# Kernel tuning notes

Hardware: AMD Instinct MI355X
Metric: run time of the kernel (lower is better)

The kernel has to match this reference:

```python
import jax, jax.numpy as jnp
import numpy as np

B, N, D, H = 8, 2048, 512, 8  # batch, seq (incl. CLS), emb_dim, heads


def setup_inputs() -> dict:
    key = jax.random.key(0)
    kx, km, k1, k2, k3, k4 = jax.random.split(key, 6)
    x = jax.random.normal(kx, (B, N, D), dtype=jnp.float32)
    # mask covers the N-1 non-CLS tokens; forward pads a leading True for CLS
    mask = jax.random.bernoulli(km, p=0.9, shape=(B, N - 1))
    s = 0.02
    Wqkv = jax.random.normal(k1, (D, 3 * D), dtype=jnp.float32) * s
    bqkv = jax.random.normal(k2, (3 * D,), dtype=jnp.float32) * s
    Wout = jax.random.normal(k3, (D, D), dtype=jnp.float32) * s
    bout = jax.random.normal(k4, (D,), dtype=jnp.float32) * s
    return {"x": x, "mask": mask, "Wqkv": Wqkv, "bqkv": bqkv,
            "Wout": Wout, "bout": bout, "num_heads": H}


def reference(x, mask, Wqkv, bqkv, Wout, bout, num_heads):
    b, n, d = x.shape
    h = num_heads
    dh = d // h
    scale = d ** (-0.5)  # NOTE: module scales by emb_dim^-0.5, not head_dim^-0.5

    qkv = x @ Wqkv + bqkv                      # [b, n, 3d]
    q, k, v = jnp.split(qkv, 3, axis=-1)
    def to_heads(t):
        return t.reshape(b, n, h, dh).transpose(0, 2, 1, 3)  # [b, h, n, dh]
    q, k, v = map(to_heads, (q, k, v))

    scores = jnp.einsum('bhqd,bhkd->bhqk', q, k) * scale     # [b, h, n, n]

    # pad leading True for CLS token, then outer-product pair mask
    m = jnp.pad(mask, ((0, 0), (1, 0)), constant_values=True)  # [b, n]
    pair = m[:, None, :, None] & m[:, None, None, :]           # [b, 1, n, n]
    neg = jnp.asarray(-1e9, dtype=scores.dtype)  # finite stand-in for -inf (avoids NaN rows)
    scores = jnp.where(pair, scores, neg)

    attn = jax.nn.softmax(scores, axis=-1)
    out = jnp.einsum('bhqk,bhkd->bhqd', attn, v)               # [b, h, n, dh]
    out = out.transpose(0, 2, 1, 3).reshape(b, n, d)
    return out @ Wout + bout
```

## Files before the change

kernel.cpp:

```cpp
#include <hip/hip_runtime.h>
#include <math.h>

#define BB  8
#define SEQ 2048
#define EMB 512
#define NH  8
#define DH  64
#define NBH (BB * NH)
#define MROWS (BB * SEQ)
#define QKV_ELEMS ((size_t)NBH * SEQ * DH)
#define MASK_ELEMS (BB * (SEQ - 1))
#define QSCALE 0.06375871307545f

typedef __attribute__((ext_vector_type(8)))  short short8;
typedef __attribute__((ext_vector_type(4)))  float float4e;
typedef __attribute__((ext_vector_type(16))) float float16e;
typedef __attribute__((ext_vector_type(4)))  unsigned int uint4e;
typedef __attribute__((ext_vector_type(2)))  unsigned int uint2e;
typedef unsigned short ushort_t;

static __device__ inline unsigned short f2bf(float f) {
    unsigned int u = __float_as_uint(f);
    unsigned int r = (u + 0x7fffu + ((u >> 16) & 1u)) >> 16;
    return (unsigned short)r;
}

static __device__ inline void gl_lds16(const unsigned short* g, unsigned short* l) {
    __builtin_amdgcn_global_load_lds(
        (const __attribute__((address_space(1))) void*)g,
        (__attribute__((address_space(3))) void*)l, 16, 0, 0);
}

#define PREP_CONV   8192
#define PREP_MASK   (PREP_CONV + 64)
#define PREP_WQ     (PREP_MASK + (1536 / 32) * (EMB / 32))
#define PREP_TOTAL  (PREP_WQ + (EMB / 32) * (EMB / 32))

__global__ __launch_bounds__(256) void prep(const float* __restrict__ x,
                                            const void* __restrict__ mraw,
                                            const float* __restrict__ Wqkv,
                                            const float* __restrict__ Wout,
                                            ushort_t* __restrict__ xb,
                                            float* __restrict__ pmf,
                                            float* __restrict__ mkl,
                                            float* __restrict__ zrow,
                                            ushort_t* __restrict__ wqt,
                                            ushort_t* __restrict__ wot) {
    __shared__ float T[32][33];
    __shared__ int flag;
    const int bid = blockIdx.x;
    const int tid = threadIdx.x;

    if (bid < PREP_CONV) {
        const size_t i = ((size_t)bid * 256 + tid) * 4;
        float4 v = *(const float4*)&x[i];
        ushort4 o;
        o.x = f2bf(v.x); o.y = f2bf(v.y); o.z = f2bf(v.z); o.w = f2bf(v.w);
        *(ushort4*)&xb[i] = o;
    } else if (bid < PREP_MASK) {
        if (tid == 0) flag = 0;
        __syncthreads();
        const unsigned int* mi = (const unsigned int*)mraw;
        int local = 0;
        for (int i = tid; i < MASK_ELEMS / 4; i += 256) {
            if (mi[i] > 1u) local = 1;
        }
        if (local) flag = 1;
        __syncthreads();
        const int isbyte = flag;
        const unsigned char* mb = (const unsigned char*)mraw;
        const int* m32 = (const int*)mraw;
        const int i = (bid - PREP_CONV) * 256 + tid;
        const int b = i >> 11, n = i & (SEQ - 1);
        int v;
        if (n == 0) v = 1;
        else {
            const int src = b * (SEQ - 1) + n - 1;
            v = isbyte ? (int)mb[src] : (m32[src] != 0 ? 1 : 0);
        }
        pmf[i] = v ? 1.0f : 0.0f;
        mkl[i] = v ? 0.0f : -1e9f;
        if (i < SEQ) zrow[i] = 0.0f;
    } else {
        const float* src;
        ushort_t* dst;
        int N, idx;
        if (bid < PREP_WQ) {
            src = Wqkv; dst = wqt; N = 1536; idx = bid - PREP_MASK;
        } else {
            src = Wout; dst = wot; N = EMB; idx = bid - PREP_WQ;
        }
        const int nb = N / 32;
        const int n0 = (idx % nb) * 32;
        const int k0 = (idx / nb) * 32;
        {
            const int r = tid >> 3, c4 = (tid & 7) * 4;
            *(float4*)&T[r][c4] = *(const float4*)&src[(size_t)(k0 + r) * N + n0 + c4];
        }
        __syncthreads();
        const int n = tid >> 3, k4 = (tid & 7) * 4;
        ushort4 hv;
        hv.x = f2bf(T[k4 + 0][n]);
        hv.y = f2bf(T[k4 + 1][n]);
        hv.z = f2bf(T[k4 + 2][n]);
        hv.w = f2bf(T[k4 + 3][n]);
        *(ushort4*)&dst[(size_t)(n0 + n) * EMB + k0 + k4] = hv;
    }
}

__global__ __launch_bounds__(256) void qkv_mfma(const ushort_t* __restrict__ xb,
                                                const ushort_t* __restrict__ wt,
                                                const float* __restrict__ bias,
                                                ushort_t* __restrict__ qb,
                                                ushort_t* __restrict__ kb,
                                                ushort_t* __restrict__ vt) {
    __shared__ __align__(16) ushort_t As[128 * 32];
    __shared__ __align__(16) ushort_t Bs[128 * 32];
    const int tid  = threadIdx.x;
    const int w    = tid >> 6;
    const int lane = tid & 63;
    const int l16  = lane & 15;
    const int quad = lane >> 4;
    const int wq   = w >> 1;
    const int wn   = w & 1;
    const int row0 = blockIdx.y * 128;
    const int col0 = blockIdx.x * 128;

    float4e acc[4][4];
    #pragma unroll
    for (int i = 0; i < 4; ++i)
        #pragma unroll
        for (int j = 0; j < 4; ++j) acc[i][j] = (float4e){0.f, 0.f, 0.f, 0.f};

    const int srow = tid >> 2;
    const int csrc = (tid & 3) ^ (srow & 3);

    for (int k0 = 0; k0 < EMB; k0 += 32) {
        #pragma unroll
        for (int s = 0; s < 2; ++s) {
            const int row = s * 64 + srow;
            gl_lds16(xb + (size_t)(row0 + row) * EMB + k0 + csrc * 8,
                     As + s * 2048 + w * 512);
            gl_lds16(wt + (size_t)(col0 + row) * EMB + k0 + csrc * 8,
                     Bs + s * 2048 + w * 512);
        }
        __syncthreads();
        short8 af[4], bf[4];
        #pragma unroll
        for (int mt = 0; mt < 4; ++mt) {
            const int rm = wq * 64 + mt * 16 + l16;
            af[mt] = *(const short8*)(As + rm * 32 + ((quad ^ (rm & 3)) * 8));
        }
        #pragma unroll
        for (int nt = 0; nt < 4; ++nt) {
            const int rn = wn * 64 + nt * 16 + l16;
            bf[nt] = *(const short8*)(Bs + rn * 32 + ((quad ^ (rn & 3)) * 8));
        }
        #pragma unroll
        for (int mt = 0; mt < 4; ++mt)
            #pragma unroll
            for (int nt = 0; nt < 4; ++nt)
                acc[mt][nt] = __builtin_amdgcn_mfma_f32_16x16x32_bf16(af[mt], bf[nt], acc[mt][nt], 0, 0, 0);
        __syncthreads();
    }

    #pragma unroll
    for (int nt = 0; nt < 4; ++nt) {
        const int cb    = col0 + wn * 64 + nt * 16;
        const int which = cb >> 9;
        const int h     = (cb >> 6) & 7;
        const int dcol  = (cb & 63) + l16;
        const float bz  = bias[cb + l16];
        if (which == 2) {
            #pragma unroll
            for (int mt = 0; mt < 4; ++mt) {
                const int rg = row0 + wq * 64 + mt * 16 + quad * 4;
                const int b = rg >> 11, n = rg & (SEQ - 1);
                ushort4 ov;
                ov.x = f2bf(acc[mt][nt][0] + bz);
                ov.y = f2bf(acc[mt][nt][1] + bz);
                ov.z = f2bf(acc[mt][nt][2] + bz);
                ov.w = f2bf(acc[mt][nt][3] + bz);
                *(ushort4*)&vt[((size_t)(b * NH + h) * DH + dcol) * SEQ + n] = ov;
            }
        } else {
            ushort_t* base = (which == 0) ? qb : kb;
            const float sc = (which == 0) ? QSCALE : 1.0f;
            #pragma unroll
            for (int mt = 0; mt < 4; ++mt) {
                #pragma unroll
                for (int i = 0; i < 4; ++i) {
                    const int rg = row0 + wq * 64 + mt * 16 + quad * 4 + i;
                    const int b = rg >> 11;
                    const int n = rg & (SEQ - 1);
                    base[((size_t)(b * NH + h) * SEQ + n) * DH + dcol] =
                        f2bf((acc[mt][nt][i] + bz) * sc);
                }
            }
        }
    }
}

__device__ inline void stage_tile(const ushort_t* kbh, const ushort_t* vbh, int kt,
                                  ushort_t* Kd, ushort_t* Vd,
                                  const int* crow, const int* csoff, int wbase) {
    #pragma unroll
    for (int j = 0; j < 4; ++j) {
        gl_lds16(kbh + (size_t)(kt * 64 + crow[j]) * DH + csoff[j],
                 Kd + (j * 128 + wbase) * 8);
        gl_lds16(vbh + (size_t)crow[j] * SEQ + kt * 64 + csoff[j],
                 Vd + (j * 128 + wbase) * 8);
    }
}

__global__ __launch_bounds__(128, 2) void attn_mfma(const ushort_t* __restrict__ qb,
                                                    const ushort_t* __restrict__ kb,
                                                    const ushort_t* __restrict__ vt,
                                                    const float* __restrict__ pmf,
                                                    const float* __restrict__ mkl,
                                                    const float* __restrict__ zrow,
                                                    ushort_t* __restrict__ ab) {
    __shared__ __align__(16) ushort_t Ks[2][64 * 64];
    __shared__ __align__(16) ushort_t Vts[2][64 * 64];
    __shared__ float lw[2][64];

    const int tid = threadIdx.x;
    const int w   = tid >> 6;
    const int lane = tid & 63;
    const int l5  = lane & 31;
    const int h   = lane >> 5;
    const int bid = blockIdx.x;
    const int ord = bid >> 3;
    const int bh  = (bid & 7) * 8 + (ord >> 4);
    const int qt  = ord & 15;
    const int b   = bh >> 3;
    const int hh  = bh & 7;
    const int q0  = qt * 128 + w * 64;

    const ushort_t* qbh = qb + (size_t)bh * SEQ * DH;
    short8 qf[2][4];
    #pragma unroll
    for (int t = 0; t < 2; ++t)
        #pragma unroll
        for (int kc = 0; kc < 4; ++kc)
            qf[t][kc] = *(const short8*)(qbh + (size_t)(q0 + t * 32 + l5) * DH + kc * 16 + h * 8);

    const float* crb[2];
    #pragma unroll
    for (int t = 0; t < 2; ++t) {
        const float mq = pmf[b * SEQ + q0 + t * 32 + l5];
        if (mq == 0.0f) {
            const short8 z8 = {0, 0, 0, 0, 0, 0, 0, 0};
            #pragma unroll
            for (int kc = 0; kc < 4; ++kc) qf[t][kc] = z8;
        }
        crb[t] = (mq != 0.0f) ? (mkl + b * SEQ) : zrow;
    }

    int crow[4], csoff[4];
    #pragma unroll
    for (int j = 0; j < 4; ++j) {
        const int c = j * 128 + tid;
        crow[j]  = c >> 3;
        csoff[j] = ((c & 7) ^ (crow[j] & 7)) * 8;
    }
    const int wbase = w * 64;
    const ushort_t* kbh = kb + (size_t)bh * SEQ * DH;
    const ushort_t* vbh = vt + (size_t)bh * DH * SEQ;

    float16e o[2][2];
    #pragma unroll
    for (int t = 0; t < 2; ++t)
        #pragma unroll
        for (int d = 0; d < 2; ++d) o[t][d] = (float16e)0.0f;
    float l_i[2] = {0.f, 0.f};

    stage_tile(kbh, vbh, 0, Ks[0], Vts[0], crow, csoff, wbase);

    for (int kt = 0; kt < 32; ++kt) {
        __syncthreads();
        const int cur = kt & 1;
        if (kt < 31)
            stage_tile(kbh, vbh, kt + 1, Ks[cur ^ 1], Vts[cur ^ 1], crow, csoff, wbase);

        #pragma unroll
        for (int s = 0; s < 2; ++s) {
            float16e st[2];
            #pragma unroll
            for (int t = 0; t < 2; ++t) {
                #pragma unroll
                for (int g2 = 0; g2 < 4; ++g2) {
                    const float4e c4 = *(const float4e*)(crb[t] + kt * 64 + s * 32 + g2 * 8 + h * 4);
                    #pragma unroll
                    for (int j = 0; j < 4; ++j)
                        st[t][g2 * 4 + j] = c4[j];
                }
            }

            const int krow = s * 32 + l5;
            short8 kf[4];
            #pragma unroll
            for (int kc = 0; kc < 4; ++kc)
                kf[kc] = *(const short8*)(Ks[cur] + krow * 64 + (((kc * 2 + h) ^ (krow & 7)) * 8));
            __builtin_amdgcn_s_setprio(1);
            #pragma unroll
            for (int kc = 0; kc < 4; ++kc) {
                st[0] = __builtin_amdgcn_mfma_f32_32x32x16_bf16(kf[kc], qf[0][kc], st[0], 0, 0, 0);
                st[1] = __builtin_amdgcn_mfma_f32_32x32x16_bf16(kf[kc], qf[1][kc], st[1], 0, 0, 0);
            }
            __builtin_amdgcn_s_setprio(0);

            short8 af[2][2];
            #pragma unroll
            for (int t = 0; t < 2; ++t) {
                unsigned int a[8];
                float lacc = 0.f;
                #pragma unroll
                for (int j = 0; j < 8; ++j) {
                    const float p0 = __builtin_amdgcn_exp2f(st[t][2 * j]);
                    const float p1 = __builtin_amdgcn_exp2f(st[t][2 * j + 1]);
                    lacc += p0 + p1;
                    a[j] = (__float_as_uint(p0) >> 16) | (__float_as_uint(p1) & 0xffff0000u);
                }
                l_i[t] += lacc;
                #pragma unroll
                for (int c = 0; c < 2; ++c) {
                    const uint2e r02 = __builtin_amdgcn_permlane32_swap(a[4 * c],     a[4 * c + 2], false, false);
                    const uint2e r13 = __builtin_amdgcn_permlane32_swap(a[4 * c + 1], a[4 * c + 3], false, false);
                    uint4e fv;
                    fv.x = r02[0];
                    fv.y = r13[0];
                    fv.z = r02[1];
                    fv.w = r13[1];
                    af[t][c] = __builtin_bit_cast(short8, fv);
                }
            }

            __builtin_amdgcn_s_setprio(1);
            #pragma unroll
            for (int c = 0; c < 2; ++c) {
                #pragma unroll
                for (int d = 0; d < 2; ++d) {
                    const int vrow = d * 32 + l5;
                    const short8 vf = *(const short8*)(Vts[cur] + vrow * 64 +
                                       (((s * 4 + c * 2 + h) ^ (vrow & 7)) * 8));
                    o[0][d] = __builtin_amdgcn_mfma_f32_32x32x16_bf16(af[0][c], vf, o[0][d], 0, 0, 0);
                    o[1][d] = __builtin_amdgcn_mfma_f32_32x32x16_bf16(af[1][c], vf, o[1][d], 0, 0, 0);
                }
            }
            __builtin_amdgcn_s_setprio(0);
        }
    }

    #pragma unroll
    for (int t = 0; t < 2; ++t) {
        const float l = l_i[t] + __shfl_xor(l_i[t], 32);
        lw[w][t * 32 + l5] = l;
    }

    ushort_t* ob = ab + ((size_t)b * SEQ + q0) * EMB + hh * DH;
    #pragma unroll
    for (int t = 0; t < 2; ++t) {
        #pragma unroll
        for (int r = 0; r < 16; ++r) {
            const int ql = (r & 3) + 8 * (r >> 2) + 4 * h;
            const float inv = 1.0f / lw[w][t * 32 + ql];
            #pragma unroll
            for (int d = 0; d < 2; ++d)
                ob[(size_t)(t * 32 + ql) * EMB + d * 32 + l5] = f2bf(o[t][d][r] * inv);
        }
    }
}

__global__ __launch_bounds__(256) void out_mfma(const ushort_t* __restrict__ ab,
                                                const ushort_t* __restrict__ wot,
                                                const float* __restrict__ bias,
                                                float* __restrict__ out) {
    __shared__ __align__(16) ushort_t As[128 * 32];
    __shared__ __align__(16) ushort_t Bs[128 * 32];
    const int tid  = threadIdx.x;
    const int w    = tid >> 6;
    const int lane = tid & 63;
    const int l16  = lane & 15;
    const int quad = lane >> 4;
    const int wq   = w >> 1;
    const int wn   = w & 1;
    const int row0 = blockIdx.y * 128;
    const int col0 = blockIdx.x * 128;

    float4e acc[4][4];
    #pragma unroll
    for (int i = 0; i < 4; ++i)
        #pragma unroll
        for (int j = 0; j < 4; ++j) acc[i][j] = (float4e){0.f, 0.f, 0.f, 0.f};

    const int srow = tid >> 2;
    const int csrc = (tid & 3) ^ (srow & 3);

    for (int k0 = 0; k0 < EMB; k0 += 32) {
        #pragma unroll
        for (int s = 0; s < 2; ++s) {
            const int row = s * 64 + srow;
            gl_lds16(ab + (size_t)(row0 + row) * EMB + k0 + csrc * 8,
                     As + s * 2048 + w * 512);
            gl_lds16(wot + (size_t)(col0 + row) * EMB + k0 + csrc * 8,
                     Bs + s * 2048 + w * 512);
        }
        __syncthreads();
        short8 af[4], bf[4];
        #pragma unroll
        for (int mt = 0; mt < 4; ++mt) {
            const int rm = wq * 64 + mt * 16 + l16;
            af[mt] = *(const short8*)(As + rm * 32 + ((quad ^ (rm & 3)) * 8));
        }
        #pragma unroll
        for (int nt = 0; nt < 4; ++nt) {
            const int rn = wn * 64 + nt * 16 + l16;
            bf[nt] = *(const short8*)(Bs + rn * 32 + ((quad ^ (rn & 3)) * 8));
        }
        #pragma unroll
        for (int mt = 0; mt < 4; ++mt)
            #pragma unroll
            for (int nt = 0; nt < 4; ++nt)
                acc[mt][nt] = __builtin_amdgcn_mfma_f32_16x16x32_bf16(af[mt], bf[nt], acc[mt][nt], 0, 0, 0);
        __syncthreads();
    }

    #pragma unroll
    for (int nt = 0; nt < 4; ++nt) {
        const int col_g = col0 + wn * 64 + nt * 16 + l16;
        const float bz = bias[col_g];
        #pragma unroll
        for (int mt = 0; mt < 4; ++mt) {
            #pragma unroll
            for (int i = 0; i < 4; ++i) {
                const int row_g = row0 + wq * 64 + mt * 16 + quad * 4 + i;
                out[(size_t)row_g * EMB + col_g] = acc[mt][nt][i] + bz;
            }
        }
    }
}

extern "C" void kernel_launch(void* const* d_in, const int* in_sizes, int n_in,
                              void* d_out, int out_size, void* d_ws, size_t ws_size,
                              hipStream_t stream) {
    const float* x    = (const float*)d_in[0];
    const void*  mask = d_in[1];
    const float* Wqkv = (const float*)d_in[2];
    const float* bqkv = (const float*)d_in[3];
    const float* Wout = (const float*)d_in[4];
    const float* bout = (const float*)d_in[5];
    float* out = (float*)d_out;

    ushort_t* xb  = (ushort_t*)d_ws;
    ushort_t* wqt = xb + (size_t)MROWS * EMB;
    ushort_t* wot = wqt + (size_t)1536 * EMB;
    ushort_t* qb  = wot + (size_t)EMB * EMB;
    ushort_t* kb  = qb + QKV_ELEMS;
    ushort_t* vt  = kb + QKV_ELEMS;
    ushort_t* ab  = vt + QKV_ELEMS;
    float*    pmf = (float*)(ab + (size_t)MROWS * EMB);
    float*    mkl = pmf + (size_t)BB * SEQ;
    float*    zrw = mkl + (size_t)BB * SEQ;

    prep<<<dim3(PREP_TOTAL), 256, 0, stream>>>(x, mask, Wqkv, Wout, xb, pmf, mkl, zrw, wqt, wot);
    qkv_mfma<<<dim3(1536 / 128, MROWS / 128), 256, 0, stream>>>(xb, wqt, bqkv, qb, kb, vt);
    attn_mfma<<<dim3(NBH * (SEQ / 128)), 128, 0, stream>>>(qb, kb, vt, pmf, mkl, zrw, ab);
    out_mfma<<<dim3(EMB / 128, MROWS / 128), 256, 0, stream>>>(ab, wot, bout, out);
}
```

Before: 250.8 us.

## Load V fragments directly to registers and prefetch K two tiles ahead

The attention kernel stops staging V through shared memory. Each lane now loads its V^T fragments straight from global memory into registers for the next tile, overlapping with the current tile's compute. K staging becomes a two-deep prefetch into the double-buffered LDS, and uses manual s_barrier and waitcnt instead of __syncthreads. The per-query mask-row pointer (zrow) is replaced by a predicate select on the mask values. This cuts LDS traffic and barrier stalls, but raises register pressure and depends on hand-placed waitcnt counts being correct.

Measured after the change: 265.6 us. 5.9% more time.

```diff
diff --git a/kernel.cpp b/kernel.cpp
--- a/kernel.cpp
+++ b/kernel.cpp
@@ -201,27 +201,32 @@
     }
 }
 
-__device__ inline void stage_tile(const ushort_t* kbh, const ushort_t* vbh, int kt,
-                                  ushort_t* Kd, ushort_t* Vd,
-                                  const int* crow, const int* csoff, int wbase) {
-    #pragma unroll
-    for (int j = 0; j < 4; ++j) {
+__device__ inline void stage_k(const ushort_t* kbh, int kt, ushort_t* Kd,
+                               const int* crow, const int* csoff, int wbase) {
+    #pragma unroll
+    for (int j = 0; j < 4; ++j)
         gl_lds16(kbh + (size_t)(kt * 64 + crow[j]) * DH + csoff[j],
                  Kd + (j * 128 + wbase) * 8);
-        gl_lds16(vbh + (size_t)crow[j] * SEQ + kt * 64 + csoff[j],
-                 Vd + (j * 128 + wbase) * 8);
-    }
-}
+}
+
+#define LOADV(KT)                                                               \
+    _Pragma("unroll")                                                           \
+    for (int s_ = 0; s_ < 2; ++s_)                                              \
+        _Pragma("unroll")                                                       \
+        for (int c_ = 0; c_ < 2; ++c_)                                          \
+            _Pragma("unroll")                                                   \
+            for (int d_ = 0; d_ < 2; ++d_)                                      \
+                vf[s_][c_][d_] = *(const short8*)(vbh +                         \
+                    (size_t)(d_ * 32 + l5) * SEQ + (KT) * 64 +                  \
+                    (s_ * 4 + c_ * 2 + h) * 8);
 
 __global__ __launch_bounds__(128, 2) void attn_mfma(const ushort_t* __restrict__ qb,
                                                     const ushort_t* __restrict__ kb,
                                                     const ushort_t* __restrict__ vt,
                                                     const float* __restrict__ pmf,
                                                     const float* __restrict__ mkl,
-                                                    const float* __restrict__ zrow,
                                                     ushort_t* __restrict__ ab) {
     __shared__ __align__(16) ushort_t Ks[2][64 * 64];
-    __shared__ __align__(16) ushort_t Vts[2][64 * 64];
     __shared__ float lw[2][64];
 
     const int tid = threadIdx.x;
@@ -245,16 +250,16 @@
         for (int kc = 0; kc < 4; ++kc)
             qf[t][kc] = *(const short8*)(qbh + (size_t)(q0 + t * 32 + l5) * DH + kc * 16 + h * 8);
 
-    const float* crb[2];
+    bool qv[2];
     #pragma unroll
     for (int t = 0; t < 2; ++t) {
         const float mq = pmf[b * SEQ + q0 + t * 32 + l5];
-        if (mq == 0.0f) {
+        qv[t] = (mq != 0.0f);
+        if (!qv[t]) {
             const short8 z8 = {0, 0, 0, 0, 0, 0, 0, 0};
             #pragma unroll
             for (int kc = 0; kc < 4; ++kc) qf[t][kc] = z8;
         }
-        crb[t] = (mq != 0.0f) ? (mkl + b * SEQ) : zrow;
     }
 
     int crow[4], csoff[4];
@@ -267,6 +272,7 @@
     const int wbase = w * 64;
     const ushort_t* kbh = kb + (size_t)bh * SEQ * DH;
     const ushort_t* vbh = vt + (size_t)bh * DH * SEQ;
+    const float*    mrow = mkl + b * SEQ;
 
     float16e o[2][2];
     #pragma unroll
@@ -275,38 +281,57 @@
         for (int d = 0; d < 2; ++d) o[t][d] = (float16e)0.0f;
     float l_i[2] = {0.f, 0.f};
 
-    stage_tile(kbh, vbh, 0, Ks[0], Vts[0], crow, csoff, wbase);
+    stage_k(kbh, 0, Ks[0], crow, csoff, wbase);
+    __builtin_amdgcn_sched_barrier(0);
+    stage_k(kbh, 1, Ks[1], crow, csoff, wbase);
+    __builtin_amdgcn_sched_barrier(0);
+    asm volatile("s_waitcnt vmcnt(4)" ::: "memory");
+    short8 vf[2][2][2];
+    LOADV(0)
 
     for (int kt = 0; kt < 32; ++kt) {
-        __syncthreads();
         const int cur = kt & 1;
-        if (kt < 31)
-            stage_tile(kbh, vbh, kt + 1, Ks[cur ^ 1], Vts[cur ^ 1], crow, csoff, wbase);
+        asm volatile("s_barrier" ::: "memory");
+
+        float4e m4[2][4];
+        #pragma unroll
+        for (int s = 0; s < 2; ++s)
+            #pragma unroll
+            for (int g2 = 0; g2 < 4; ++g2)
+                m4[s][g2] = *(const float4e*)(mrow + kt * 64 + s * 32 + g2 * 8 + h * 4);
+
+        short8 kf[2][4];
+        #pragma unroll
+        for (int s = 0; s < 2; ++s)
+            #pragma unroll
+            for (int kc = 0; kc < 4; ++kc) {
+                const int krow = s * 32 + l5;
+                kf[s][kc] = *(const short8*)(Ks[cur] + krow * 64 + (((kc * 2 + h) ^ (krow & 7)) * 8));
+            }
+        asm volatile("s_waitcnt lgkmcnt(0)" ::: "memory");
+        __builtin_amdgcn_sched_barrier(0);
+        asm volatile("s_barrier" ::: "memory");
+
+        if (kt < 30)
+            stage_k(kbh, kt + 2, Ks[cur], crow, csoff, wbase);
 
         #pragma unroll
         for (int s = 0; s < 2; ++s) {
             float16e st[2];
             #pragma unroll
-            for (int t = 0; t < 2; ++t) {
+            for (int g2 = 0; g2 < 4; ++g2)
                 #pragma unroll
-                for (int g2 = 0; g2 < 4; ++g2) {
-                    const float4e c4 = *(const float4e*)(crb[t] + kt * 64 + s * 32 + g2 * 8 + h * 4);
-                    #pragma unroll
-                    for (int j = 0; j < 4; ++j)
-                        st[t][g2 * 4 + j] = c4[j];
+                for (int j = 0; j < 4; ++j) {
+                    const float v = m4[s][g2][j];
+                    st[0][g2 * 4 + j] = qv[0] ? v : 0.0f;
+                    st[1][g2 * 4 + j] = qv[1] ? v : 0.0f;
                 }
-            }
-
-            const int krow = s * 32 + l5;
-            short8 kf[4];
-            #pragma unroll
-            for (int kc = 0; kc < 4; ++kc)
-                kf[kc] = *(const short8*)(Ks[cur] + krow * 64 + (((kc * 2 + h) ^ (krow & 7)) * 8));
+
             __builtin_amdgcn_s_setprio(1);
             #pragma unroll
             for (int kc = 0; kc < 4; ++kc) {
-                st[0] = __builtin_amdgcn_mfma_f32_32x32x16_bf16(kf[kc], qf[0][kc], st[0], 0, 0, 0);
-                st[1] = __builtin_amdgcn_mfma_f32_32x32x16_bf16(kf[kc], qf[1][kc], st[1], 0, 0, 0);
+                st[0] = __builtin_amdgcn_mfma_f32_32x32x16_bf16(kf[s][kc], qf[0][kc], st[0], 0, 0, 0);
+                st[1] = __builtin_amdgcn_mfma_f32_32x32x16_bf16(kf[s][kc], qf[1][kc], st[1], 0, 0, 0);
             }
             __builtin_amdgcn_s_setprio(0);
 
@@ -341,14 +366,15 @@
             for (int c = 0; c < 2; ++c) {
                 #pragma unroll
                 for (int d = 0; d < 2; ++d) {
-                    const int vrow = d * 32 + l5;
-                    const short8 vf = *(const short8*)(Vts[cur] + vrow * 64 +
-                                       (((s * 4 + c * 2 + h) ^ (vrow & 7)) * 8));
-                    o[0][d] = __builtin_amdgcn_mfma_f32_32x32x16_bf16(af[0][c], vf, o[0][d], 0, 0, 0);
-                    o[1][d] = __builtin_amdgcn_mfma_f32_32x32x16_bf16(af[1][c], vf, o[1][d], 0, 0, 0);
+                    o[0][d] = __builtin_amdgcn_mfma_f32_32x32x16_bf16(af[0][c], vf[s][c][d], o[0][d], 0, 0, 0);
+                    o[1][d] = __builtin_amdgcn_mfma_f32_32x32x16_bf16(af[1][c], vf[s][c][d], o[1][d], 0, 0, 0);
                 }
             }
             __builtin_amdgcn_s_setprio(0);
+        }
+
+        if (kt < 31) {
+            LOADV(kt + 1)
         }
     }
 
@@ -465,6 +491,6 @@
 
     prep<<<dim3(PREP_TOTAL), 256, 0, stream>>>(x, mask, Wqkv, Wout, xb, pmf, mkl, zrw, wqt, wot);
     qkv_mfma<<<dim3(1536 / 128, MROWS / 128), 256, 0, stream>>>(xb, wqt, bqkv, qb, kb, vt);
-    attn_mfma<<<dim3(NBH * (SEQ / 128)), 128, 0, stream>>>(qb, kb, vt, pmf, mkl, zrw, ab);
+    attn_mfma<<<dim3(NBH * (SEQ / 128)), 128, 0, stream>>>(qb, kb, vt, pmf, mkl, ab);
     out_mfma<<<dim3(EMB / 128, MROWS / 128), 256, 0, stream>>>(ab, wot, bout, out);
 }
```

## Split attention key range across two wave pairs and merge partial sums via LDS

Applied to the files above, without the earlier changes.

The attention block grows from 2 to 4 waves. Each pair of waves handles half of the 2048 keys, using 32-key tiles and its own double-buffered K/V staging in LDS. The partial outputs and row sums of the second half are written to shared memory and added by the first half before normalisation. This is meant to raise occupancy and parallelism per query tile (split-K flash-decoding style), in exchange for an extra LDS reduction, more syncs and smaller tiles per iteration.

Result: slower. 677.0 us (+169.9%).

```diff
diff --git a/kernel.cpp b/kernel.cpp
--- a/kernel.cpp
+++ b/kernel.cpp
@@ -201,41 +201,44 @@
     }
 }
 
-__device__ inline void stage_tile(const ushort_t* kbh, const ushort_t* vbh, int kt,
-                                  ushort_t* Kd, ushort_t* Vd,
-                                  const int* crow, const int* csoff, int wbase) {
-    #pragma unroll
-    for (int j = 0; j < 4; ++j) {
-        gl_lds16(kbh + (size_t)(kt * 64 + crow[j]) * DH + csoff[j],
-                 Kd + (j * 128 + wbase) * 8);
-        gl_lds16(vbh + (size_t)crow[j] * SEQ + kt * 64 + csoff[j],
-                 Vd + (j * 128 + wbase) * 8);
-    }
-}
-
-__global__ __launch_bounds__(128, 2) void attn_mfma(const ushort_t* __restrict__ qb,
+__device__ inline void stage_half(const ushort_t* kbh, const ushort_t* vbh,
+                                  int keybase, ushort_t* Kd, ushort_t* Vd,
+                                  int wp, int lane) {
+    #pragma unroll
+    for (int j = 0; j < 2; ++j) {
+        const int c = j * 128 + wp * 64 + lane;
+        const int r = c >> 3;
+        const int q = (c & 7) ^ (r & 7);
+        gl_lds16(kbh + (size_t)(keybase + r) * DH + q * 8,
+                 Kd + (size_t)(j * 128 + wp * 64) * 8);
+        gl_lds16(vbh + (size_t)((q >> 2) * 32 + r) * SEQ + keybase + (q & 3) * 8,
+                 Vd + (size_t)(j * 128 + wp * 64) * 8);
+    }
+}
+
+__global__ __launch_bounds__(256, 4) void attn_mfma(const ushort_t* __restrict__ qb,
                                                     const ushort_t* __restrict__ kb,
                                                     const ushort_t* __restrict__ vt,
                                                     const float* __restrict__ pmf,
                                                     const float* __restrict__ mkl,
-                                                    const float* __restrict__ zrow,
                                                     ushort_t* __restrict__ ab) {
-    __shared__ __align__(16) ushort_t Ks[2][64 * 64];
-    __shared__ __align__(16) ushort_t Vts[2][64 * 64];
-    __shared__ float lw[2][64];
-
-    const int tid = threadIdx.x;
-    const int w   = tid >> 6;
+    __shared__ __align__(16) ushort_t smem[16384];
+    __shared__ float Lx[2][2][64];
+
+    const int tid  = threadIdx.x;
+    const int w    = tid >> 6;
+    const int half = w >> 1;
+    const int wp   = w & 1;
     const int lane = tid & 63;
-    const int l5  = lane & 31;
-    const int h   = lane >> 5;
+    const int l5   = lane & 31;
+    const int h    = lane >> 5;
     const int bid = blockIdx.x;
     const int ord = bid >> 3;
     const int bh  = (bid & 7) * 8 + (ord >> 4);
     const int qt  = ord & 15;
     const int b   = bh >> 3;
     const int hh  = bh & 7;
-    const int q0  = qt * 128 + w * 64;
+    const int q0  = qt * 128 + wp * 64;
 
     const ushort_t* qbh = qb + (size_t)bh * SEQ * DH;
     short8 qf[2][4];
@@ -245,28 +248,21 @@
         for (int kc = 0; kc < 4; ++kc)
             qf[t][kc] = *(const short8*)(qbh + (size_t)(q0 + t * 32 + l5) * DH + kc * 16 + h * 8);
 
-    const float* crb[2];
+    bool qv[2];
     #pragma unroll
     for (int t = 0; t < 2; ++t) {
         const float mq = pmf[b * SEQ + q0 + t * 32 + l5];
-        if (mq == 0.0f) {
+        qv[t] = (mq != 0.0f);
+        if (!qv[t]) {
             const short8 z8 = {0, 0, 0, 0, 0, 0, 0, 0};
             #pragma unroll
             for (int kc = 0; kc < 4; ++kc) qf[t][kc] = z8;
         }
-        crb[t] = (mq != 0.0f) ? (mkl + b * SEQ) : zrow;
-    }
-
-    int crow[4], csoff[4];
-    #pragma unroll
-    for (int j = 0; j < 4; ++j) {
-        const int c = j * 128 + tid;
-        crow[j]  = c >> 3;
-        csoff[j] = ((c & 7) ^ (crow[j] & 7)) * 8;
-    }
-    const int wbase = w * 64;
+    }
+
     const ushort_t* kbh = kb + (size_t)bh * SEQ * DH;
     const ushort_t* vbh = vt + (size_t)bh * DH * SEQ;
+    const float*    mrow = mkl + b * SEQ + half * 1024;
 
     float16e o[2][2];
     #pragma unroll
@@ -275,99 +271,126 @@
         for (int d = 0; d < 2; ++d) o[t][d] = (float16e)0.0f;
     float l_i[2] = {0.f, 0.f};
 
-    stage_tile(kbh, vbh, 0, Ks[0], Vts[0], crow, csoff, wbase);
+    ushort_t* const Kbuf[2] = {smem + (half * 2 + 0) * 2 * 2048,
+                               smem + (half * 2 + 1) * 2 * 2048};
+    ushort_t* const Vbuf[2] = {Kbuf[0] + 2048, Kbuf[1] + 2048};
+
+    stage_half(kbh, vbh, half * 1024, Kbuf[0], Vbuf[0], wp, lane);
 
     for (int kt = 0; kt < 32; ++kt) {
         __syncthreads();
         const int cur = kt & 1;
         if (kt < 31)
-            stage_tile(kbh, vbh, kt + 1, Ks[cur ^ 1], Vts[cur ^ 1], crow, csoff, wbase);
-
-        #pragma unroll
-        for (int s = 0; s < 2; ++s) {
-            float16e st[2];
-            #pragma unroll
-            for (int t = 0; t < 2; ++t) {
+            stage_half(kbh, vbh, half * 1024 + (kt + 1) * 32,
+                       Kbuf[cur ^ 1], Vbuf[cur ^ 1], wp, lane);
+
+        float4e m4[4];
+        #pragma unroll
+        for (int g2 = 0; g2 < 4; ++g2)
+            m4[g2] = *(const float4e*)(mrow + kt * 32 + g2 * 8 + h * 4);
+
+        float16e st[2];
+        #pragma unroll
+        for (int g2 = 0; g2 < 4; ++g2)
+            #pragma unroll
+            for (int j = 0; j < 4; ++j) {
+                const float v = m4[g2][j];
+                st[0][g2 * 4 + j] = qv[0] ? v : 0.0f;
+                st[1][g2 * 4 + j] = qv[1] ? v : 0.0f;
+            }
+
+        short8 kf[4];
+        #pragma unroll
+        for (int kc = 0; kc < 4; ++kc)
+            kf[kc] = *(const short8*)(Kbuf[cur] + l5 * 64 + (((kc * 2 + h) ^ (l5 & 7)) * 8));
+        __builtin_amdgcn_s_setprio(1);
+        #pragma unroll
+        for (int kc = 0; kc < 4; ++kc) {
+            st[0] = __builtin_amdgcn_mfma_f32_32x32x16_bf16(kf[kc], qf[0][kc], st[0], 0, 0, 0);
+            st[1] = __builtin_amdgcn_mfma_f32_32x32x16_bf16(kf[kc], qf[1][kc], st[1], 0, 0, 0);
+        }
+        __builtin_amdgcn_s_setprio(0);
+
+        short8 af[2][2];
+        #pragma unroll
+        for (int t = 0; t < 2; ++t) {
+            unsigned int a[8];
+            float lacc = 0.f;
+            #pragma unroll
+            for (int j = 0; j < 8; ++j) {
+                const float p0 = __builtin_amdgcn_exp2f(st[t][2 * j]);
+                const float p1 = __builtin_amdgcn_exp2f(st[t][2 * j + 1]);
+                lacc += p0 + p1;
+                a[j] = (__float_as_uint(p0) >> 16) | (__float_as_uint(p1) & 0xffff0000u);
+            }
+            l_i[t] += lacc;
+            #pragma unroll
+            for (int c = 0; c < 2; ++c) {
+                const uint2e r02 = __builtin_amdgcn_permlane32_swap(a[4 * c],     a[4 * c + 2], false, false);
+                const uint2e r13 = __builtin_amdgcn_permlane32_swap(a[4 * c + 1], a[4 * c + 3], false, false);
+                uint4e fv;
+                fv.x = r02[0];
+                fv.y = r13[0];
+                fv.z = r02[1];
+                fv.w = r13[1];
+                af[t][c] = __builtin_bit_cast(short8, fv);
+            }
+        }
+
+        __builtin_amdgcn_s_setprio(1);
+        #pragma unroll
+        for (int c = 0; c < 2; ++c) {
+            #pragma unroll
+            for (int d = 0; d < 2; ++d) {
+                const short8 vf = *(const short8*)(Vbuf[cur] + l5 * 64 +
+                                   (((d * 4 + c * 2 + h) ^ (l5 & 7)) * 8));
+                o[0][d] = __builtin_amdgcn_mfma_f32_32x32x16_bf16(af[0][c], vf, o[0][d], 0, 0, 0);
+                o[1][d] = __builtin_amdgcn_mfma_f32_32x32x16_bf16(af[1][c], vf, o[1][d], 0, 0, 0);
+            }
+        }
+        __builtin_amdgcn_s_setprio(0);
+    }
+
+    float lt[2];
+    #pragma unroll
+    for (int t = 0; t < 2; ++t)
+        lt[t] = l_i[t] + __shfl_xor(l_i[t], 32);
+
+    __syncthreads();
+    float* Ox = (float*)smem;
+    if (half == 1) {
+        #pragma unroll
+        for (int t = 0; t < 2; ++t) {
+            Lx[1][wp][t * 32 + l5] = lt[t];
+            #pragma unroll
+            for (int r = 0; r < 16; ++r) {
+                const int ql = (r & 3) + 8 * (r >> 2) + 4 * h;
                 #pragma unroll
-                for (int g2 = 0; g2 < 4; ++g2) {
-                    const float4e c4 = *(const float4e*)(crb[t] + kt * 64 + s * 32 + g2 * 8 + h * 4);
-                    #pragma unroll
-                    for (int j = 0; j < 4; ++j)
-                        st[t][g2 * 4 + j] = c4[j];
-                }
-            }
-
-            const int krow = s * 32 + l5;
-            short8 kf[4];
-            #pragma unroll
-            for (int kc = 0; kc < 4; ++kc)
-                kf[kc] = *(const short8*)(Ks[cur] + krow * 64 + (((kc * 2 + h) ^ (krow & 7)) * 8));
-            __builtin_amdgcn_s_setprio(1);
-            #pragma unroll
-            for (int kc = 0; kc < 4; ++kc) {
-                st[0] = __builtin_amdgcn_mfma_f32_32x32x16_bf16(kf[kc], qf[0][kc], st[0], 0, 0, 0);
-                st[1] = __builtin_amdgcn_mfma_f32_32x32x16_bf16(kf[kc], qf[1][kc], st[1], 0, 0, 0);
-            }
-            __builtin_amdgcn_s_setprio(0);
-
-            short8 af[2][2];
-            #pragma unroll
-            for (int t = 0; t < 2; ++t) {
-                unsigned int a[8];
-                float lacc = 0.f;
-                #pragma unroll
-                for (int j = 0; j < 8; ++j) {
-                    const float p0 = __builtin_amdgcn_exp2f(st[t][2 * j]);
-                    const float p1 = __builtin_amdgcn_exp2f(st[t][2 * j + 1]);
-                    lacc += p0 + p1;
-                    a[j] = (__float_as_uint(p0) >> 16) | (__float_as_uint(p1) & 0xffff0000u);
-                }
-                l_i[t] += lacc;
-                #pragma unroll
-                for (int c = 0; c < 2; ++c) {
-                    const uint2e r02 = __builtin_amdgcn_permlane32_swap(a[4 * c],     a[4 * c + 2], false, false);
-                    const uint2e r13 = __builtin_amdgcn_permlane32_swap(a[4 * c + 1], a[4 * c + 3], false, false);
-                    uint4e fv;
-                    fv.x = r02[0];
-                    fv.y = r13[0];
-                    fv.z = r02[1];
-                    fv.w = r13[1];
-                    af[t][c] = __builtin_bit_cast(short8, fv);
-                }
-            }
-
-            __builtin_amdgcn_s_setprio(1);
-            #pragma unroll
-            for (int c = 0; c < 2; ++c) {
+                for (int d = 0; d < 2; ++d)
+                    Ox[(size_t)(wp * 64 + t * 32 + ql) * 64 + d * 32 + l5] = o[t][d][r];
+            }
+        }
+    } else {
+        #pragma unroll
+        for (int t = 0; t < 2; ++t)
+            Lx[0][wp][t * 32 + l5] = lt[t];
+    }
+    __syncthreads();
+    if (half == 0) {
+        ushort_t* ob = ab + ((size_t)b * SEQ + q0) * EMB + hh * DH;
+        #pragma unroll
+        for (int t = 0; t < 2; ++t) {
+            #pragma unroll
+            for (int r = 0; r < 16; ++r) {
+                const int ql = (r & 3) + 8 * (r >> 2) + 4 * h;
+                const float inv = 1.0f / (Lx[0][wp][t * 32 + ql] + Lx[1][wp][t * 32 + ql]);
                 #pragma unroll
                 for (int d = 0; d < 2; ++d) {
-                    const int vrow = d * 32 + l5;
-                    const short8 vf = *(const short8*)(Vts[cur] + vrow * 64 +
-                                       (((s * 4 + c * 2 + h) ^ (vrow & 7)) * 8));
-                    o[0][d] = __builtin_amdgcn_mfma_f32_32x32x16_bf16(af[0][c], vf, o[0][d], 0, 0, 0);
-                    o[1][d] = __builtin_amdgcn_mfma_f32_32x32x16_bf16(af[1][c], vf, o[1][d], 0, 0, 0);
+                    const float val = o[t][d][r] +
+                        Ox[(size_t)(wp * 64 + t * 32 + ql) * 64 + d * 32 + l5];
+                    ob[(size_t)(t * 32 + ql) * EMB + d * 32 + l5] = f2bf(val * inv);
                 }
             }
-            __builtin_amdgcn_s_setprio(0);
-        }
-    }
-
-    #pragma unroll
-    for (int t = 0; t < 2; ++t) {
-        const float l = l_i[t] + __shfl_xor(l_i[t], 32);
-        lw[w][t * 32 + l5] = l;
-    }
-
-    ushort_t* ob = ab + ((size_t)b * SEQ + q0) * EMB + hh * DH;
-    #pragma unroll
-    for (int t = 0; t < 2; ++t) {
-        #pragma unroll
-        for (int r = 0; r < 16; ++r) {
-            const int ql = (r & 3) + 8 * (r >> 2) + 4 * h;
-            const float inv = 1.0f / lw[w][t * 32 + ql];
-            #pragma unroll
-            for (int d = 0; d < 2; ++d)
-                ob[(size_t)(t * 32 + ql) * EMB + d * 32 + l5] = f2bf(o[t][d][r] * inv);
         }
     }
 }
@@ -465,6 +488,6 @@
 
     prep<<<dim3(PREP_TOTAL), 256, 0, stream>>>(x, mask, Wqkv, Wout, xb, pmf, mkl, zrw, wqt, wot);
     qkv_mfma<<<dim3(1536 / 128, MROWS / 128), 256, 0, stream>>>(xb, wqt, bqkv, qb, kb, vt);
-    attn_mfma<<<dim3(NBH * (SEQ / 128)), 128, 0, stream>>>(qb, kb, vt, pmf, mkl, zrw, ab);
+    attn_mfma<<<dim3(NBH * (SEQ / 128)), 256, 0, stream>>>(qb, kb, vt, pmf, mkl, ab);
     out_mfma<<<dim3(EMB / 128, MROWS / 128), 256, 0, stream>>>(ab, wot, bout, out);
 }
```

## Double GEMM K-tile to 64 and remap blocks for XCD-local L2 reuse

Applied to the files above, without the earlier changes.

Both projection GEMMs (QKV and output) now stage a 64-wide K slice per iteration instead of 32, with an 8-way XOR swizzle, which halves the number of barrier pairs per tile. The 2D grid becomes a 1D grid whose block index is decoded so that consecutive blocks (bid & 7 selects the chiplet) work on contiguous row groups. The intent is for blocks sharing A rows to land on the same XCD L2. The cost is doubled LDS per block (32 KB), which may lower occupancy.

New measurement: 248.9 us. Within noise of the previous version (-0.8%).

```diff
diff --git a/kernel.cpp b/kernel.cpp
--- a/kernel.cpp
+++ b/kernel.cpp
@@ -114,8 +114,8 @@
                                                 ushort_t* __restrict__ qb,
                                                 ushort_t* __restrict__ kb,
                                                 ushort_t* __restrict__ vt) {
-    __shared__ __align__(16) ushort_t As[128 * 32];
-    __shared__ __align__(16) ushort_t Bs[128 * 32];
+    __shared__ __align__(16) ushort_t As[128 * 64];
+    __shared__ __align__(16) ushort_t Bs[128 * 64];
     const int tid  = threadIdx.x;
     const int w    = tid >> 6;
     const int lane = tid & 63;
@@ -123,8 +123,13 @@
     const int quad = lane >> 4;
     const int wq   = w >> 1;
     const int wn   = w & 1;
-    const int row0 = blockIdx.y * 128;
-    const int col0 = blockIdx.x * 128;
+    const int bid  = blockIdx.x;
+    const int c    = bid & 7;
+    const int r    = bid >> 3;
+    const int mloc = r / 12;
+    const int nblk = r - mloc * 12;
+    const int row0 = (c * 16 + mloc) * 128;
+    const int col0 = nblk * 128;
 
     float4e acc[4][4];
     #pragma unroll
@@ -132,35 +137,38 @@
         #pragma unroll
         for (int j = 0; j < 4; ++j) acc[i][j] = (float4e){0.f, 0.f, 0.f, 0.f};
 
-    const int srow = tid >> 2;
-    const int csrc = (tid & 3) ^ (srow & 3);
-
-    for (int k0 = 0; k0 < EMB; k0 += 32) {
-        #pragma unroll
-        for (int s = 0; s < 2; ++s) {
-            const int row = s * 64 + srow;
+    const int srow = tid >> 3;
+    const int csrc = (tid & 7) ^ (srow & 7);
+
+    for (int k0 = 0; k0 < EMB; k0 += 64) {
+        #pragma unroll
+        for (int s = 0; s < 4; ++s) {
+            const int row = s * 32 + srow;
             gl_lds16(xb + (size_t)(row0 + row) * EMB + k0 + csrc * 8,
                      As + s * 2048 + w * 512);
             gl_lds16(wt + (size_t)(col0 + row) * EMB + k0 + csrc * 8,
                      Bs + s * 2048 + w * 512);
         }
         __syncthreads();
-        short8 af[4], bf[4];
-        #pragma unroll
-        for (int mt = 0; mt < 4; ++mt) {
-            const int rm = wq * 64 + mt * 16 + l16;
-            af[mt] = *(const short8*)(As + rm * 32 + ((quad ^ (rm & 3)) * 8));
-        }
-        #pragma unroll
-        for (int nt = 0; nt < 4; ++nt) {
-            const int rn = wn * 64 + nt * 16 + l16;
-            bf[nt] = *(const short8*)(Bs + rn * 32 + ((quad ^ (rn & 3)) * 8));
-        }
-        #pragma unroll
-        for (int mt = 0; mt < 4; ++mt)
-            #pragma unroll
-            for (int nt = 0; nt < 4; ++nt)
-                acc[mt][nt] = __builtin_amdgcn_mfma_f32_16x16x32_bf16(af[mt], bf[nt], acc[mt][nt], 0, 0, 0);
+        #pragma unroll
+        for (int kk = 0; kk < 2; ++kk) {
+            short8 af[4], bf[4];
+            #pragma unroll
+            for (int mt = 0; mt < 4; ++mt) {
+                const int rm = wq * 64 + mt * 16 + l16;
+                af[mt] = *(const short8*)(As + rm * 64 + (((kk * 4 + quad) ^ (rm & 7)) * 8));
+            }
+            #pragma unroll
+            for (int nt = 0; nt < 4; ++nt) {
+                const int rn = wn * 64 + nt * 16 + l16;
+                bf[nt] = *(const short8*)(Bs + rn * 64 + (((kk * 4 + quad) ^ (rn & 7)) * 8));
+            }
+            #pragma unroll
+            for (int mt = 0; mt < 4; ++mt)
+                #pragma unroll
+                for (int nt = 0; nt < 4; ++nt)
+                    acc[mt][nt] = __builtin_amdgcn_mfma_f32_16x16x32_bf16(af[mt], bf[nt], acc[mt][nt], 0, 0, 0);
+        }
         __syncthreads();
     }
 
@@ -376,8 +384,8 @@
                                                 const ushort_t* __restrict__ wot,
                                                 const float* __restrict__ bias,
                                                 float* __restrict__ out) {
-    __shared__ __align__(16) ushort_t As[128 * 32];
-    __shared__ __align__(16) ushort_t Bs[128 * 32];
+    __shared__ __align__(16) ushort_t As[128 * 64];
+    __shared__ __align__(16) ushort_t Bs[128 * 64];
     const int tid  = threadIdx.x;
     const int w    = tid >> 6;
     const int lane = tid & 63;
@@ -385,8 +393,13 @@
     const int quad = lane >> 4;
     const int wq   = w >> 1;
     const int wn   = w & 1;
-    const int row0 = blockIdx.y * 128;
-    const int col0 = blockIdx.x * 128;
+    const int bid  = blockIdx.x;
+    const int c    = bid & 7;
+    const int r    = bid >> 3;
+    const int mloc = r >> 2;
+    const int nblk = r & 3;
+    const int row0 = (c * 16 + mloc) * 128;
+    const int col0 = nblk * 128;
 
     float4e acc[4][4];
     #pragma unroll
@@ -394,35 +407,38 @@
         #pragma unroll
         for (int j = 0; j < 4; ++j) acc[i][j] = (float4e){0.f, 0.f, 0.f, 0.f};
 
-    const int srow = tid >> 2;
-    const int csrc = (tid & 3) ^ (srow & 3);
-
-    for (int k0 = 0; k0 < EMB; k0 += 32) {
-        #pragma unroll
-        for (int s = 0; s < 2; ++s) {
-            const int row = s * 64 + srow;
+    const int srow = tid >> 3;
+    const int csrc = (tid & 7) ^ (srow & 7);
+
+    for (int k0 = 0; k0 < EMB; k0 += 64) {
+        #pragma unroll
+        for (int s = 0; s < 4; ++s) {
+            const int row = s * 32 + srow;
             gl_lds16(ab + (size_t)(row0 + row) * EMB + k0 + csrc * 8,
                      As + s * 2048 + w * 512);
             gl_lds16(wot + (size_t)(col0 + row) * EMB + k0 + csrc * 8,
                      Bs + s * 2048 + w * 512);
         }
         __syncthreads();
-        short8 af[4], bf[4];
-        #pragma unroll
-        for (int mt = 0; mt < 4; ++mt) {
-            const int rm = wq * 64 + mt * 16 + l16;
-            af[mt] = *(const short8*)(As + rm * 32 + ((quad ^ (rm & 3)) * 8));
-        }
-        #pragma unroll
-        for (int nt = 0; nt < 4; ++nt) {
-            const int rn = wn * 64 + nt * 16 + l16;
-            bf[nt] = *(const short8*)(Bs + rn * 32 + ((quad ^ (rn & 3)) * 8));
-        }
-        #pragma unroll
-        for (int mt = 0; mt < 4; ++mt)
-            #pragma unroll
-            for (int nt = 0; nt < 4; ++nt)
-                acc[mt][nt] = __builtin_amdgcn_mfma_f32_16x16x32_bf16(af[mt], bf[nt], acc[mt][nt], 0, 0, 0);
+        #pragma unroll
+        for (int kk = 0; kk < 2; ++kk) {
+            short8 af[4], bf[4];
+            #pragma unroll
+            for (int mt = 0; mt < 4; ++mt) {
+                const int rm = wq * 64 + mt * 16 + l16;
+                af[mt] = *(const short8*)(As + rm * 64 + (((kk * 4 + quad) ^ (rm & 7)) * 8));
+            }
+            #pragma unroll
+            for (int nt = 0; nt < 4; ++nt) {
+                const int rn = wn * 64 + nt * 16 + l16;
+                bf[nt] = *(const short8*)(Bs + rn * 64 + (((kk * 4 + quad) ^ (rn & 7)) * 8));
+            }
+            #pragma unroll
+            for (int mt = 0; mt < 4; ++mt)
+                #pragma unroll
+                for (int nt = 0; nt < 4; ++nt)
+                    acc[mt][nt] = __builtin_amdgcn_mfma_f32_16x16x32_bf16(af[mt], bf[nt], acc[mt][nt], 0, 0, 0);
+        }
         __syncthreads();
     }
 
@@ -464,7 +480,7 @@
     float*    zrw = mkl + (size_t)BB * SEQ;
 
     prep<<<dim3(PREP_TOTAL), 256, 0, stream>>>(x, mask, Wqkv, Wout, xb, pmf, mkl, zrw, wqt, wot);
-    qkv_mfma<<<dim3(1536 / 128, MROWS / 128), 256, 0, stream>>>(xb, wqt, bqkv, qb, kb, vt);
+    qkv_mfma<<<dim3(1536), 256, 0, stream>>>(xb, wqt, bqkv, qb, kb, vt);
     attn_mfma<<<dim3(NBH * (SEQ / 128)), 128, 0, stream>>>(qb, kb, vt, pmf, mkl, zrw, ab);
-    out_mfma<<<dim3(EMB / 128, MROWS / 128), 256, 0, stream>>>(ab, wot, bout, out);
-}
+    out_mfma<<<dim3(512), 256, 0, stream>>>(ab, wot, bout, out);
+}
```
